# Performance work log

Measured on AMD Instinct MI355X. Metric: run time of the kernel, lower is better.

Reference implementation:

```python
import jax, jax.numpy as jnp
import numpy as np


def setup_inputs() -> dict:
    key = jax.random.key(0)
    ks = jax.random.split(key, 9)
    bs, nf, h, w = 4, 512, 64, 64
    c8 = nf // 8
    sc = 1.0 / np.sqrt(nf)
    return {
        "x": jax.random.normal(ks[0], (bs, nf, h, w), dtype=jnp.float32),
        "Wq": jax.random.normal(ks[1], (c8, nf), dtype=jnp.float32) * sc,
        "bq": jax.random.normal(ks[2], (c8,), dtype=jnp.float32) * 0.01,
        "Wk": jax.random.normal(ks[3], (c8, nf), dtype=jnp.float32) * sc,
        "bk": jax.random.normal(ks[4], (c8,), dtype=jnp.float32) * 0.01,
        "Wv": jax.random.normal(ks[5], (nf, nf), dtype=jnp.float32) * sc,
        "bv": jax.random.normal(ks[6], (nf,), dtype=jnp.float32) * 0.01,
        "alpha": jax.random.normal(ks[7], (1,), dtype=jnp.float32) * 0.1,
    }


def reference(x, Wq, bq, Wk, bk, Wv, bv, alpha):
    bs, nf, h, w = x.shape
    hw = h * w
    xf = x.reshape(bs, nf, hw)  # flatten spatial; 1x1 conv == channel matmul
    q = jnp.einsum('oc,bcn->bon', Wq, xf) + bq[:, None]  # (bs, c8, hw)
    k = jnp.einsum('oc,bcn->bon', Wk, xf) + bk[:, None]  # (bs, c8, hw)
    v = jnp.einsum('oc,bcn->bon', Wv, xf) + bv[:, None]  # (bs, nf, hw)
    # scores[b, i, j] = key_i . query_j ; softmax over j (queries)
    scores = jnp.einsum('bci,bcj->bij', k, q)  # (bs, hw, hw)
    attn = jax.nn.softmax(scores, axis=-1)
    # out[b, c, i] = sum_j v[b, c, j] * attn[b, i, j]
    out = jnp.einsum('bcj,bij->bci', v, attn).reshape(bs, nf, h, w)
    return x + alpha * out
```

## Files before the change

### kernel.cpp

```cpp
#include <hip/hip_runtime.h>

#define BS 4
#define NF 512
#define HW 4096
#define C8 64
#define TI 64

typedef unsigned short bfu;
typedef __attribute__((ext_vector_type(8))) short bf16x8;
typedef __attribute__((ext_vector_type(4))) float f32x4;

static __device__ __forceinline__ bfu f2bu(float v) {
    union { unsigned int u; float f; } c; c.f = v;
    unsigned int u = c.u;
    u = u + 0x7FFFu + ((u >> 16) & 1u);
    return (bfu)(u >> 16);
}

static __device__ __forceinline__ void gload16(const void* g, void* l) {
    __builtin_amdgcn_global_load_lds(
        (const __attribute__((address_space(1))) unsigned int*)g,
        (__attribute__((address_space(3))) unsigned int*)l,
        16, 0, 0);
}

__global__ __launch_bounds__(256) void k0_xt(const float* __restrict__ x, bfu* __restrict__ xt)
{
    __shared__ float T[64][68];
    const int t  = threadIdx.x;
    const int n0 = blockIdx.x * 64;
    const int c0 = blockIdx.y * 64;
    const int b  = blockIdx.z;

    #pragma unroll
    for (int u = 0; u < 4; u++) {
        int f4 = u * 256 + t;
        int cc = f4 >> 4;
        int n4 = (f4 & 15) << 2;
        float4 v = *(const float4*)(x + ((size_t)(b * NF + c0 + cc)) * HW + n0 + n4);
        *(float4*)&T[cc][n4] = v;
    }
    __syncthreads();
    #pragma unroll
    for (int u = 0; u < 2; u++) {
        int e8 = u * 256 + t;
        int nn = e8 >> 3;
        int c8 = (e8 & 7) << 3;
        union { int4 i4; bfu h[8]; } pk;
        #pragma unroll
        for (int q = 0; q < 8; q++) pk.h[q] = f2bu(T[c8 + q][nn]);
        *(int4*)(xt + ((size_t)(b * HW + n0 + nn)) * NF + c0 + c8) = pk.i4;
    }
}

__global__ __launch_bounds__(256) void k0_w(const float* __restrict__ Wq, const float* __restrict__ bq,
                                            const float* __restrict__ Wk, const float* __restrict__ bk,
                                            const float* __restrict__ Wv, const float* __restrict__ bv,
                                            bfu* __restrict__ Wb, float* __restrict__ bcat)
{
    const int o = blockIdx.x;
    const int t = threadIdx.x;
    const float* src; float bias;
    if (o < 64)       { src = Wq + (size_t)o * NF;          bias = bq[o]; }
    else if (o < 128) { src = Wk + (size_t)(o - 64) * NF;   bias = bk[o - 64]; }
    else              { src = Wv + (size_t)(o - 128) * NF;  bias = bv[o - 128]; }
    float2 v = *(const float2*)(src + t * 2);
    Wb[(size_t)o * NF + t * 2 + 0] = f2bu(v.x);
    Wb[(size_t)o * NF + t * 2 + 1] = f2bu(v.y);
    if (t == 0) bcat[o] = bias;
}

__global__ __launch_bounds__(256) void k1_proj(const bfu* __restrict__ Wb, const float* __restrict__ bcat,
                                               const bfu* __restrict__ xt,
                                               bfu* __restrict__ Qb, bfu* __restrict__ Kb, bfu* __restrict__ Vb)
{
    __shared__ bfu As[128 * 64];
    __shared__ bfu Bs[128 * 64];
    const int t  = threadIdx.x;
    const int o0 = blockIdx.x * 128;
    const int n0 = blockIdx.y * 128;
    const int b  = blockIdx.z;
    const int lane = t & 63, wv = t >> 6;
    const int wm = wv & 1, wn = wv >> 1;
    const int l15 = lane & 15, quad = lane >> 4;

    const int srow = t >> 3;
    const int scol = (t & 7) * 8;

    const bfu* gA = Wb + ((size_t)(o0 + srow)) * NF + scol;
    const bfu* gB = xt + ((size_t)(b * HW + n0 + srow)) * NF + scol;
    bfu* lA = As + t * 8;
    bfu* lB = Bs + t * 8;

    f32x4 acc[4][4];
    #pragma unroll
    for (int m = 0; m < 4; m++)
        #pragma unroll
        for (int n = 0; n < 4; n++) acc[m][n] = (f32x4){0.f, 0.f, 0.f, 0.f};

    for (int c0 = 0; c0 < NF; c0 += 64) {
        __syncthreads();
        #pragma unroll
        for (int p = 0; p < 4; p++) {
            gload16(gA + (size_t)(p * 32) * NF + c0, lA + p * 2048);
            gload16(gB + (size_t)(p * 32) * NF + c0, lB + p * 2048);
        }
        __syncthreads();

        #pragma unroll
        for (int kk = 0; kk < 64; kk += 32) {
            bf16x8 Af[4], Bf[4];
            #pragma unroll
            for (int m = 0; m < 4; m++)
                Af[m] = *(const bf16x8*)(As + (wm * 64 + m * 16 + l15) * 64 + kk + quad * 8);
            #pragma unroll
            for (int n = 0; n < 4; n++)
                Bf[n] = *(const bf16x8*)(Bs + (wn * 64 + n * 16 + l15) * 64 + kk + quad * 8);
            #pragma unroll
            for (int m = 0; m < 4; m++)
                #pragma unroll
                for (int n = 0; n < 4; n++)
                    acc[m][n] = __builtin_amdgcn_mfma_f32_16x16x32_bf16(Af[m], Bf[n], acc[m][n], 0, 0, 0);
        }
    }

    #pragma unroll
    for (int mt = 0; mt < 4; mt++)
        #pragma unroll
        for (int nt = 0; nt < 4; nt++)
            #pragma unroll
            for (int r = 0; r < 4; r++) {
                int go = o0 + wm * 64 + mt * 16 + quad * 4 + r;
                int n  = n0 + wn * 64 + nt * 16 + l15;
                float val = acc[mt][nt][r] + bcat[go];
                if (go < 64)
                    Qb[((size_t)(b * HW + n)) * C8 + go] = f2bu(val);
                else if (go < 128)
                    Kb[((size_t)(b * HW + n)) * C8 + (go - 64)] = f2bu(val);
                else
                    Vb[((size_t)(b * NF + (go - 128))) * HW + n] = f2bu(val);
            }
}

__global__ __launch_bounds__(512, 2) void k23_fused(const bfu* __restrict__ Kb, const bfu* __restrict__ Qb,
                                                    const bfu* __restrict__ Vb,
                                                    const float* __restrict__ x, const float* __restrict__ alpha,
                                                    float* __restrict__ out)
{
    __shared__ bfu   Vs[2][512 * 64];
    __shared__ bfu   Ps[TI * 72];
    __shared__ float LSum[8][2][16];
    __shared__ float Scale[TI];

    const int t = threadIdx.x;
    const int lane = t & 63, w = t >> 6;
    const int l15 = lane & 15, quad = lane >> 4;
    const int jq  = w & 3;
    const int iqb = (w >> 2) * 32;
    const int cw  = w * 64;

    const int d    = blockIdx.x;
    const int xcd  = d & 7;
    const int slot = d >> 3;
    const int b    = xcd >> 1;
    const int i0   = ((xcd & 1) * 32 + slot) * TI;

    const bfu* kp0 = Kb + ((size_t)(b * HW + i0 + iqb + l15)) * C8 + quad * 8;
    const bfu* kp1 = kp0 + (size_t)16 * C8;
    const bf16x8 Kf00 = *(const bf16x8*)kp0;
    const bf16x8 Kf01 = *(const bf16x8*)(kp0 + 32);
    const bf16x8 Kf10 = *(const bf16x8*)kp1;
    const bf16x8 Kf11 = *(const bf16x8*)(kp1 + 32);

    const int srow = t >> 3, sslot = t & 7;
    const bfu* gV = Vb + ((size_t)(b * NF + srow)) * HW + ((sslot ^ (srow & 7)) * 8);

    const bfu* qbase = Qb + ((size_t)(b * HW + jq * 16 + l15)) * C8 + quad * 8;

    const int r7  = l15 & 7;
    const int sl0 = (quad ^ r7) * 8;
    const int sl1 = ((quad + 4) ^ r7) * 8;

    f32x4 acc[4][4];
    #pragma unroll
    for (int mt = 0; mt < 4; mt++)
        #pragma unroll
        for (int nt = 0; nt < 4; nt++) acc[mt][nt] = (f32x4){0.f, 0.f, 0.f, 0.f};
    float rs0 = 0.f, rs1 = 0.f;
    bf16x8 Aq[2][2];

    {
        bfu* lv = &Vs[0][t * 8];
        #pragma unroll
        for (int p = 0; p < 8; p++) gload16(gV + (size_t)(p * 64) * HW, lv + p * 4096);
        Aq[0][0] = *(const bf16x8*)qbase;
        Aq[0][1] = *(const bf16x8*)(qbase + 32);
    }

#define K23_ITER(q, pc, pn)                                                                    \
  {                                                                                            \
    const int jn = (((q) + 1) & 63) * 64;                                                      \
                          \
    bfu* lv = &Vs[pn][t * 8];                                                                  \
    _Pragma("unroll")                                                                          \
    for (int p = 0; p < 8; p++)                                                                \
        gload16(gV + (size_t)(p * 64) * HW + jn, lv + p * 4096);                               \
    {                                                                                          \
        const bfu* qpn = qbase + (size_t)jn * C8;                                              \
        Aq[pn][0] = *(const bf16x8*)qpn;                                                       \
        Aq[pn][1] = *(const bf16x8*)(qpn + 32);                                                \
    }                                                                                          \
       \
    asm volatile("s_waitcnt vmcnt(10)" ::: "memory");                                          \
    __builtin_amdgcn_sched_barrier(0);                                                         \
                                    \
    {                                                                                          \
        f32x4 s0 = (f32x4){0.f,0.f,0.f,0.f}, s1 = (f32x4){0.f,0.f,0.f,0.f};                    \
        s0 = __builtin_amdgcn_mfma_f32_16x16x32_bf16(Aq[pc][0], Kf00, s0, 0, 0, 0);            \
        s0 = __builtin_amdgcn_mfma_f32_16x16x32_bf16(Aq[pc][1], Kf01, s0, 0, 0, 0);            \
        s1 = __builtin_amdgcn_mfma_f32_16x16x32_bf16(Aq[pc][0], Kf10, s1, 0, 0, 0);            \
        s1 = __builtin_amdgcn_mfma_f32_16x16x32_bf16(Aq[pc][1], Kf11, s1, 0, 0, 0);            \
        float e0 = __expf(s0[0]), e1 = __expf(s0[1]), e2 = __expf(s0[2]), e3 = __expf(s0[3]);  \
        float f0 = __expf(s1[0]), f1 = __expf(s1[1]), f2 = __expf(s1[2]), f3 = __expf(s1[3]);  \
        rs0 += (e0 + e1) + (e2 + e3);                                                          \
        rs1 += (f0 + f1) + (f2 + f3);                                                          \
        uint2 pk0, pk1;                                                                        \
        pk0.x = (unsigned)f2bu(e0) | ((unsigned)f2bu(e1) << 16);                               \
        pk0.y = (unsigned)f2bu(e2) | ((unsigned)f2bu(e3) << 16);                               \
        pk1.x = (unsigned)f2bu(f0) | ((unsigned)f2bu(f1) << 16);                               \
        pk1.y = (unsigned)f2bu(f2) | ((unsigned)f2bu(f3) << 16);                               \
        *(uint2*)(Ps + (iqb + l15)      * 72 + jq * 16 + quad * 4) = pk0;                      \
        *(uint2*)(Ps + (iqb + 16 + l15) * 72 + jq * 16 + quad * 4) = pk1;                      \
    }                                                                                          \
    asm volatile("s_waitcnt lgkmcnt(0)" ::: "memory");                                         \
    __builtin_amdgcn_sched_barrier(0);                                                         \
    __builtin_amdgcn_s_barrier();                       \
                                               \
    {                                                                                          \
        bf16x8 Pf[4][2];                                                                       \
        _Pragma("unroll")                                                                      \
        for (int nt = 0; nt < 4; nt++) {                                                       \
            Pf[nt][0] = *(const bf16x8*)(Ps + (nt * 16 + l15) * 72 + quad * 8);                \
            Pf[nt][1] = *(const bf16x8*)(Ps + (nt * 16 + l15) * 72 + 32 + quad * 8);           \
        }                                                                                      \
        __builtin_amdgcn_s_setprio(1);                                                         \
        _Pragma("unroll")                                                                      \
        for (int mt = 0; mt < 4; mt++) {                                                       \
            const bfu* vrow = &Vs[pc][(cw + mt * 16 + l15) * 64];                              \
            bf16x8 V0 = *(const bf16x8*)(vrow + sl0);                                          \
            bf16x8 V1 = *(const bf16x8*)(vrow + sl1);                                          \
            _Pragma("unroll")                                                                  \
            for (int nt = 0; nt < 4; nt++) {                                                   \
                acc[mt][nt] = __builtin_amdgcn_mfma_f32_16x16x32_bf16(V0, Pf[nt][0], acc[mt][nt], 0, 0, 0); \
                acc[mt][nt] = __builtin_amdgcn_mfma_f32_16x16x32_bf16(V1, Pf[nt][1], acc[mt][nt], 0, 0, 0); \
            }                                                                                  \
        }                                                                                      \
        __builtin_amdgcn_s_setprio(0);                                                         \
    }                                                                                          \
    __builtin_amdgcn_sched_barrier(0);                                                         \
    __builtin_amdgcn_s_barrier();    \
  }

    for (int qq = 0; qq < 32; qq++) {
        K23_ITER(2 * qq,     0, 1)
        K23_ITER(2 * qq + 1, 1, 0)
    }
#undef K23_ITER

    float sred0 = rs0, sred1 = rs1;
    sred0 += __shfl_xor(sred0, 16, 64);
    sred0 += __shfl_xor(sred0, 32, 64);
    sred1 += __shfl_xor(sred1, 16, 64);
    sred1 += __shfl_xor(sred1, 32, 64);
    if (quad == 0) { LSum[w][0][l15] = sred0; LSum[w][1][l15] = sred1; }
    __syncthreads();
    if (t < TI) {
        int u = t >> 5, s = (t >> 4) & 1, il = t & 15;
        float L = (LSum[u * 4 + 0][s][il] + LSum[u * 4 + 1][s][il])
                + (LSum[u * 4 + 2][s][il] + LSum[u * 4 + 3][s][il]);
        Scale[t] = alpha[0] / L;
    }
    __syncthreads();

    #pragma unroll
    for (int nt = 0; nt < 4; nt++) {
        float sc = Scale[nt * 16 + l15];
        int i = i0 + nt * 16 + l15;
        #pragma unroll
        for (int mt = 0; mt < 4; mt++)
            #pragma unroll
            for (int r = 0; r < 4; r++) {
                int c = cw + mt * 16 + quad * 4 + r;
                size_t idx = ((size_t)(b * NF + c)) * HW + i;
                out[idx] = x[idx] + sc * acc[mt][nt][r];
            }
    }
}

extern "C" void kernel_launch(void* const* d_in, const int* in_sizes, int n_in,
                              void* d_out, int out_size, void* d_ws, size_t ws_size,
                              hipStream_t stream)
{
    const float* x     = (const float*)d_in[0];
    const float* Wq    = (const float*)d_in[1];
    const float* bq    = (const float*)d_in[2];
    const float* Wk    = (const float*)d_in[3];
    const float* bk    = (const float*)d_in[4];
    const float* Wv    = (const float*)d_in[5];
    const float* bv    = (const float*)d_in[6];
    const float* alpha = (const float*)d_in[7];
    float* out = (float*)d_out;

    char* ws = (char*)d_ws;
    bfu*   xt   = (bfu*)(ws);
    bfu*   Wb   = (bfu*)(ws + (16u << 20));
    float* bcat = (float*)(ws + (17u << 20));
    bfu*   Qb   = (bfu*)(ws + (18u << 20));
    bfu*   Kb   = (bfu*)(ws + (20u << 20));
    bfu*   Vb   = (bfu*)(ws + (22u << 20));

    k0_xt<<<dim3(HW / 64, NF / 64, BS), 256, 0, stream>>>(x, xt);
    k0_w<<<dim3(640), 256, 0, stream>>>(Wq, bq, Wk, bk, Wv, bv, Wb, bcat);
    k1_proj<<<dim3(5, HW / 128, BS), 256, 0, stream>>>(Wb, bcat, xt, Qb, Kb, Vb);
    k23_fused<<<dim3(HW / TI * BS), 512, 0, stream>>>(Kb, Qb, Vb, x, alpha, out);
}
```

Measured before the change: 264.9 us.

## Split attention over channel halves, double-buffer projection GEMM, swizzle LDS tiles

The fused attention kernel now splits the 512 output channels into two 256-channel blocks, doubling the grid and halving the V tile in LDS, with launch bounds raised to target four blocks per CU. The cost is that each block recomputes the QK scores and softmax for its channel half. The projection GEMM gains double-buffered LDS staging with XOR-swizzled layouts and a vectorized packed-bf16 epilogue for Q/K. The transpose kernel swizzles its shared tile to reduce bank conflicts, and bf16 packing switches to the hardware v_cvt_pk_bf16_f32 instruction.

```diff
diff --git a/kernel.cpp b/kernel.cpp
--- a/kernel.cpp
+++ b/kernel.cpp
@@ -17,6 +17,12 @@
     return (bfu)(u >> 16);
 }
 
+static __device__ __forceinline__ unsigned int cvt_pk_bf16(float lo, float hi) {
+    unsigned int r;
+    asm("v_cvt_pk_bf16_f32 %0, %1, %2" : "=v"(r) : "v"(lo), "v"(hi));
+    return r;
+}
+
 static __device__ __forceinline__ void gload16(const void* g, void* l) {
     __builtin_amdgcn_global_load_lds(
         (const __attribute__((address_space(1))) unsigned int*)g,
@@ -38,7 +44,7 @@
         int cc = f4 >> 4;
         int n4 = (f4 & 15) << 2;
         float4 v = *(const float4*)(x + ((size_t)(b * NF + c0 + cc)) * HW + n0 + n4);
-        *(float4*)&T[cc][n4] = v;
+        *(float4*)&T[cc][n4 ^ (((cc >> 3) & 3) << 2)] = v;
     }
     __syncthreads();
     #pragma unroll
@@ -48,7 +54,8 @@
         int c8 = (e8 & 7) << 3;
         union { int4 i4; bfu h[8]; } pk;
         #pragma unroll
-        for (int q = 0; q < 8; q++) pk.h[q] = f2bu(T[c8 + q][nn]);
+        for (int q = 0; q < 8; q++)
+            pk.h[q] = f2bu(T[c8 + q][nn ^ ((((c8 + q) >> 3) & 3) << 2)]);
         *(int4*)(xt + ((size_t)(b * HW + n0 + nn)) * NF + c0 + c8) = pk.i4;
     }
 }
@@ -74,8 +81,8 @@
                                                const bfu* __restrict__ xt,
                                                bfu* __restrict__ Qb, bfu* __restrict__ Kb, bfu* __restrict__ Vb)
 {
-    __shared__ bfu As[128 * 64];
-    __shared__ bfu Bs[128 * 64];
+    __shared__ bfu As[2][128 * 64];
+    __shared__ bfu Bs[2][128 * 64];
     const int t  = threadIdx.x;
     const int o0 = blockIdx.x * 128;
     const int n0 = blockIdx.y * 128;
@@ -83,14 +90,15 @@
     const int lane = t & 63, wv = t >> 6;
     const int wm = wv & 1, wn = wv >> 1;
     const int l15 = lane & 15, quad = lane >> 4;
+    const int r7  = l15 & 7;
+    const int sl0 = (quad ^ r7) * 8;
+    const int sl1 = ((quad + 4) ^ r7) * 8;
 
     const int srow = t >> 3;
-    const int scol = (t & 7) * 8;
-
-    const bfu* gA = Wb + ((size_t)(o0 + srow)) * NF + scol;
-    const bfu* gB = xt + ((size_t)(b * HW + n0 + srow)) * NF + scol;
-    bfu* lA = As + t * 8;
-    bfu* lB = Bs + t * 8;
+    const int scolz = ((t & 7) ^ (srow & 7)) * 8;
+
+    const bfu* gA = Wb + ((size_t)(o0 + srow)) * NF + scolz;
+    const bfu* gB = xt + ((size_t)(b * HW + n0 + srow)) * NF + scolz;
 
     f32x4 acc[4][4];
     #pragma unroll
@@ -98,56 +106,95 @@
         #pragma unroll
         for (int n = 0; n < 4; n++) acc[m][n] = (f32x4){0.f, 0.f, 0.f, 0.f};
 
-    for (int c0 = 0; c0 < NF; c0 += 64) {
-        __syncthreads();
-        #pragma unroll
-        for (int p = 0; p < 4; p++) {
-            gload16(gA + (size_t)(p * 32) * NF + c0, lA + p * 2048);
-            gload16(gB + (size_t)(p * 32) * NF + c0, lB + p * 2048);
-        }
-        __syncthreads();
-
-        #pragma unroll
-        for (int kk = 0; kk < 64; kk += 32) {
-            bf16x8 Af[4], Bf[4];
+#define K1_STAGE(buf, c0)                                                       \
+    _Pragma("unroll")                                                           \
+    for (int p = 0; p < 4; p++) {                                               \
+        gload16(gA + (size_t)(p * 32) * NF + (c0), &As[buf][t * 8 + p * 2048]); \
+        gload16(gB + (size_t)(p * 32) * NF + (c0), &Bs[buf][t * 8 + p * 2048]); \
+    }
+
+#define K1_COMPUTE(pc)                                                                      \
+    {                                                                                       \
+        bf16x8 Af0[4], Af1[4], Bf0[4], Bf1[4];                                              \
+        _Pragma("unroll")                                                                   \
+        for (int m = 0; m < 4; m++) {                                                       \
+            const bfu* ar = &As[pc][(wm * 64 + m * 16 + l15) * 64];                         \
+            Af0[m] = *(const bf16x8*)(ar + sl0);                                            \
+            Af1[m] = *(const bf16x8*)(ar + sl1);                                            \
+        }                                                                                   \
+        _Pragma("unroll")                                                                   \
+        for (int n = 0; n < 4; n++) {                                                       \
+            const bfu* br = &Bs[pc][(wn * 64 + n * 16 + l15) * 64];                         \
+            Bf0[n] = *(const bf16x8*)(br + sl0);                                            \
+            Bf1[n] = *(const bf16x8*)(br + sl1);                                            \
+        }                                                                                   \
+        __builtin_amdgcn_s_setprio(1);                                                      \
+        _Pragma("unroll")                                                                   \
+        for (int m = 0; m < 4; m++)                                                         \
+            _Pragma("unroll")                                                               \
+            for (int n = 0; n < 4; n++) {                                                   \
+                acc[m][n] = __builtin_amdgcn_mfma_f32_16x16x32_bf16(Af0[m], Bf0[n], acc[m][n], 0, 0, 0); \
+                acc[m][n] = __builtin_amdgcn_mfma_f32_16x16x32_bf16(Af1[m], Bf1[n], acc[m][n], 0, 0, 0); \
+            }                                                                               \
+        __builtin_amdgcn_s_setprio(0);                                                      \
+    }
+
+    K1_STAGE(0, 0)
+    for (int it = 0; it < 7; it++) {
+        const int pc = it & 1;
+        K1_STAGE(pc ^ 1, (it + 1) * 64)
+        asm volatile("s_waitcnt vmcnt(8)" ::: "memory");
+        __builtin_amdgcn_sched_barrier(0);
+        __builtin_amdgcn_s_barrier();
+        K1_COMPUTE(pc)
+        __builtin_amdgcn_sched_barrier(0);
+        __builtin_amdgcn_s_barrier();
+    }
+    asm volatile("s_waitcnt vmcnt(0)" ::: "memory");
+    __builtin_amdgcn_sched_barrier(0);
+    __builtin_amdgcn_s_barrier();
+    K1_COMPUTE(1)
+#undef K1_STAGE
+#undef K1_COMPUTE
+
+    if (o0 == 0) {
+        #pragma unroll
+        for (int mt = 0; mt < 4; mt++)
             #pragma unroll
-            for (int m = 0; m < 4; m++)
-                Af[m] = *(const bf16x8*)(As + (wm * 64 + m * 16 + l15) * 64 + kk + quad * 8);
+            for (int nt = 0; nt < 4; nt++) {
+                int goq = wm * 64 + mt * 16 + quad * 4;
+                int n   = n0 + wn * 64 + nt * 16 + l15;
+                float v0 = acc[mt][nt][0] + bcat[goq + 0];
+                float v1 = acc[mt][nt][1] + bcat[goq + 1];
+                float v2 = acc[mt][nt][2] + bcat[goq + 2];
+                float v3 = acc[mt][nt][3] + bcat[goq + 3];
+                int2 pk;
+                pk.x = (int)cvt_pk_bf16(v0, v1);
+                pk.y = (int)cvt_pk_bf16(v2, v3);
+                if (wm == 0) *(int2*)(Qb + ((size_t)(b * HW + n)) * C8 + goq)      = pk;
+                else         *(int2*)(Kb + ((size_t)(b * HW + n)) * C8 + goq - 64) = pk;
+            }
+    } else {
+        #pragma unroll
+        for (int mt = 0; mt < 4; mt++)
             #pragma unroll
-            for (int n = 0; n < 4; n++)
-                Bf[n] = *(const bf16x8*)(Bs + (wn * 64 + n * 16 + l15) * 64 + kk + quad * 8);
-            #pragma unroll
-            for (int m = 0; m < 4; m++)
+            for (int nt = 0; nt < 4; nt++)
                 #pragma unroll
-                for (int n = 0; n < 4; n++)
-                    acc[m][n] = __builtin_amdgcn_mfma_f32_16x16x32_bf16(Af[m], Bf[n], acc[m][n], 0, 0, 0);
-        }
-    }
-
-    #pragma unroll
-    for (int mt = 0; mt < 4; mt++)
-        #pragma unroll
-        for (int nt = 0; nt < 4; nt++)
-            #pragma unroll
-            for (int r = 0; r < 4; r++) {
-                int go = o0 + wm * 64 + mt * 16 + quad * 4 + r;
-                int n  = n0 + wn * 64 + nt * 16 + l15;
-                float val = acc[mt][nt][r] + bcat[go];
-                if (go < 64)
-                    Qb[((size_t)(b * HW + n)) * C8 + go] = f2bu(val);
-                else if (go < 128)
-                    Kb[((size_t)(b * HW + n)) * C8 + (go - 64)] = f2bu(val);
-                else
+                for (int r = 0; r < 4; r++) {
+                    int go = o0 + wm * 64 + mt * 16 + quad * 4 + r;
+                    int n  = n0 + wn * 64 + nt * 16 + l15;
+                    float val = acc[mt][nt][r] + bcat[go];
                     Vb[((size_t)(b * NF + (go - 128))) * HW + n] = f2bu(val);
-            }
-}
-
-__global__ __launch_bounds__(512, 2) void k23_fused(const bfu* __restrict__ Kb, const bfu* __restrict__ Qb,
+                }
+    }
+}
+
+__global__ __launch_bounds__(512, 4) void k23_fused(const bfu* __restrict__ Kb, const bfu* __restrict__ Qb,
                                                     const bfu* __restrict__ Vb,
                                                     const float* __restrict__ x, const float* __restrict__ alpha,
                                                     float* __restrict__ out)
 {
-    __shared__ bfu   Vs[2][512 * 64];
+    __shared__ bfu   Vs[2][256 * 64];
     __shared__ bfu   Ps[TI * 72];
     __shared__ float LSum[8][2][16];
     __shared__ float Scale[TI];
@@ -157,13 +204,12 @@
     const int l15 = lane & 15, quad = lane >> 4;
     const int jq  = w & 3;
     const int iqb = (w >> 2) * 32;
-    const int cw  = w * 64;
 
     const int d    = blockIdx.x;
     const int xcd  = d & 7;
-    const int slot = d >> 3;
     const int b    = xcd >> 1;
-    const int i0   = ((xcd & 1) * 32 + slot) * TI;
+    const int cblk = xcd & 1;
+    const int i0   = (d >> 3) * TI;
 
     const bfu* kp0 = Kb + ((size_t)(b * HW + i0 + iqb + l15)) * C8 + quad * 8;
     const bfu* kp1 = kp0 + (size_t)16 * C8;
@@ -173,7 +219,7 @@
     const bf16x8 Kf11 = *(const bf16x8*)(kp1 + 32);
 
     const int srow = t >> 3, sslot = t & 7;
-    const bfu* gV = Vb + ((size_t)(b * NF + srow)) * HW + ((sslot ^ (srow & 7)) * 8);
+    const bfu* gV = Vb + ((size_t)(b * NF + cblk * 256 + srow)) * HW + ((sslot ^ (srow & 7)) * 8);
 
     const bfu* qbase = Qb + ((size_t)(b * HW + jq * 16 + l15)) * C8 + quad * 8;
 
@@ -181,18 +227,18 @@
     const int sl0 = (quad ^ r7) * 8;
     const int sl1 = ((quad + 4) ^ r7) * 8;
 
-    f32x4 acc[4][4];
-    #pragma unroll
-    for (int mt = 0; mt < 4; mt++)
+    f32x4 acc[2][4];
+    #pragma unroll
+    for (int mt = 0; mt < 2; mt++)
         #pragma unroll
         for (int nt = 0; nt < 4; nt++) acc[mt][nt] = (f32x4){0.f, 0.f, 0.f, 0.f};
     float rs0 = 0.f, rs1 = 0.f;
     bf16x8 Aq[2][2];
 
     {
-        bfu* lv = &Vs[0][t * 8];
-        #pragma unroll
-        for (int p = 0; p < 8; p++) gload16(gV + (size_t)(p * 64) * HW, lv + p * 4096);
+        #pragma unroll
+        for (int p = 0; p < 4; p++)
+            gload16(gV + (size_t)(p * 64) * HW, &Vs[0][t * 8 + p * 4096]);
         Aq[0][0] = *(const bf16x8*)qbase;
         Aq[0][1] = *(const bf16x8*)(qbase + 32);
     }
@@ -201,17 +247,16 @@
   {                                                                                            \
     const int jn = (((q) + 1) & 63) * 64;                                                      \
                           \
-    bfu* lv = &Vs[pn][t * 8];                                                                  \
     _Pragma("unroll")                                                                          \
-    for (int p = 0; p < 8; p++)                                                                \
-        gload16(gV + (size_t)(p * 64) * HW + jn, lv + p * 4096);                               \
+    for (int p = 0; p < 4; p++)                                                                \
+        gload16(gV + (size_t)(p * 64) * HW + jn, &Vs[pn][t * 8 + p * 4096]);                   \
     {                                                                                          \
         const bfu* qpn = qbase + (size_t)jn * C8;                                              \
         Aq[pn][0] = *(const bf16x8*)qpn;                                                       \
         Aq[pn][1] = *(const bf16x8*)(qpn + 32);                                                \
     }                                                                                          \
-       \
-    asm volatile("s_waitcnt vmcnt(10)" ::: "memory");                                          \
+        \
+    asm volatile("s_waitcnt vmcnt(6)" ::: "memory");                                           \
     __builtin_amdgcn_sched_barrier(0);                                                         \
                                     \
     {                                                                                          \
@@ -225,10 +270,8 @@
         rs0 += (e0 + e1) + (e2 + e3);                                                          \
         rs1 += (f0 + f1) + (f2 + f3);                                                          \
         uint2 pk0, pk1;                                                                        \
-        pk0.x = (unsigned)f2bu(e0) | ((unsigned)f2bu(e1) << 16);                               \
-        pk0.y = (unsigned)f2bu(e2) | ((unsigned)f2bu(e3) << 16);                               \
-        pk1.x = (unsigned)f2bu(f0) | ((unsigned)f2bu(f1) << 16);                               \
-        pk1.y = (unsigned)f2bu(f2) | ((unsigned)f2bu(f3) << 16);                               \
+        pk0.x = cvt_pk_bf16(e0, e1);  pk0.y = cvt_pk_bf16(e2, e3);                             \
+        pk1.x = cvt_pk_bf16(f0, f1);  pk1.y = cvt_pk_bf16(f2, f3);                             \
         *(uint2*)(Ps + (iqb + l15)      * 72 + jq * 16 + quad * 4) = pk0;                      \
         *(uint2*)(Ps + (iqb + 16 + l15) * 72 + jq * 16 + quad * 4) = pk1;                      \
     }                                                                                          \
@@ -245,8 +288,8 @@
         }                                                                                      \
         __builtin_amdgcn_s_setprio(1);                                                         \
         _Pragma("unroll")                                                                      \
-        for (int mt = 0; mt < 4; mt++) {                                                       \
-            const bfu* vrow = &Vs[pc][(cw + mt * 16 + l15) * 64];                              \
+        for (int mt = 0; mt < 2; mt++) {                                                       \
+            const bfu* vrow = &Vs[pc][(w * 32 + mt * 16 + l15) * 64];                          \
             bf16x8 V0 = *(const bf16x8*)(vrow + sl0);                                          \
             bf16x8 V1 = *(const bf16x8*)(vrow + sl1);                                          \
             _Pragma("unroll")                                                                  \
@@ -287,10 +330,10 @@
         float sc = Scale[nt * 16 + l15];
         int i = i0 + nt * 16 + l15;
         #pragma unroll
-        for (int mt = 0; mt < 4; mt++)
+        for (int mt = 0; mt < 2; mt++)
             #pragma unroll
             for (int r = 0; r < 4; r++) {
-                int c = cw + mt * 16 + quad * 4 + r;
+                int c = cblk * 256 + w * 32 + mt * 16 + quad * 4 + r;
                 size_t idx = ((size_t)(b * NF + c)) * HW + i;
                 out[idx] = x[idx] + sc * acc[mt][nt][r];
             }
@@ -322,5 +365,5 @@
     k0_xt<<<dim3(HW / 64, NF / 64, BS), 256, 0, stream>>>(x, xt);
     k0_w<<<dim3(640), 256, 0, stream>>>(Wq, bq, Wk, bk, Wv, bv, Wb, bcat);
     k1_proj<<<dim3(5, HW / 128, BS), 256, 0, stream>>>(Wb, bcat, xt, Qb, Kb, Vb);
-    k23_fused<<<dim3(HW / TI * BS), 512, 0, stream>>>(Kb, Qb, Vb, x, alpha, out);
-}
+    k23_fused<<<dim3(HW / TI * BS * 2), 512, 0, stream>>>(Kb, Qb, Vb, x, alpha, out);
+}
```

After: 240.6 us. -9.2%, faster.
